# Kernel tuning notes

Measured on AMD Instinct MI355X. Metric: run time of the kernel, lower is better.

Reference implementation:

```python
import jax, jax.numpy as jnp
import numpy as np

N = 100000
E = 1600000
IN_DIM, HID, OUT, HEADS, EDGE_DIM = 64, 32, 32, 4, 1


def setup_inputs() -> dict:
    key = jax.random.key(0)
    ks = jax.random.split(key, 24)
    p = lambda k, shape: (jax.random.normal(k, shape, dtype=jnp.float32) * 0.1)
    inp = {
        "x": jax.random.normal(ks[0], (N, IN_DIM), dtype=jnp.float32),
        "edge_index": jax.random.randint(ks[1], (2, E), 0, N, dtype=jnp.int32),
        "edge_attr": jax.random.uniform(ks[2], (E, EDGE_DIM), dtype=jnp.float32),
        # BatchNorm1d(edge_dim), eval mode
        "bn_gamma": jnp.ones((EDGE_DIM,), jnp.float32),
        "bn_beta": jnp.zeros((EDGE_DIM,), jnp.float32),
        "bn_mean": jnp.zeros((EDGE_DIM,), jnp.float32),
        "bn_var": jnp.ones((EDGE_DIM,), jnp.float32),
        # GATConv layer 1: in_dim -> hidden, heads=4, concat
        "W1": p(ks[3], (IN_DIM, HEADS * HID)),
        "as1": p(ks[4], (HEADS, HID)),
        "ad1": p(ks[5], (HEADS, HID)),
        "We1": p(ks[6], (EDGE_DIM, HEADS * HID)),
        "ae1": p(ks[7], (HEADS, HID)),
        "b1": jnp.zeros((HEADS * HID,), jnp.float32),
        # GATConv layer 2: heads*hidden -> out, heads=1, no concat
        "W2": p(ks[8], (HEADS * HID, OUT)),
        "as2": p(ks[9], (1, OUT)),
        "ad2": p(ks[10], (1, OUT)),
        "We2": p(ks[11], (EDGE_DIM, OUT)),
        "ae2": p(ks[12], (1, OUT)),
        "b2": jnp.zeros((OUT,), jnp.float32),
        # feature decoder MLP
        "Wd1": p(ks[13], (OUT, HID)),
        "bd1": jnp.zeros((HID,), jnp.float32),
        "Wd2": p(ks[14], (HID, IN_DIM)),
        "bd2": jnp.zeros((IN_DIM,), jnp.float32),
    }
    return inp


def gat_layer(x, src, dst, e, W, a_src, a_dst, We, a_e, b, heads, out_ch, concat):
    n = x.shape[0]
    h = (x @ W).reshape(n, heads, out_ch)                     # [N,H,C]
    alpha_src = (h * a_src).sum(-1)                           # [N,H]
    alpha_dst = (h * a_dst).sum(-1)                           # [N,H]
    he = (e @ We).reshape(-1, heads, out_ch)                  # [E,H,C]
    alpha = alpha_src[src] + alpha_dst[dst] + (he * a_e).sum(-1)  # [E,H]
    alpha = jax.nn.leaky_relu(alpha, 0.2)
    # segment softmax over destination node
    amax = jax.ops.segment_max(alpha, dst, num_segments=n)
    amax = jnp.where(jnp.isfinite(amax), amax, 0.0)
    ex = jnp.exp(alpha - amax[dst])
    denom = jax.ops.segment_sum(ex, dst, num_segments=n)
    att = ex / (denom[dst] + 1e-16)                           # [E,H]
    msg = h[src] * att[:, :, None]                            # [E,H,C]
    out = jax.ops.segment_sum(msg, dst, num_segments=n)       # [N,H,C]
    out = out.reshape(n, heads * out_ch) if concat else out.mean(axis=1)
    return out + b


def reference(x, edge_index, edge_attr, bn_gamma, bn_beta, bn_mean, bn_var,
              W1, as1, ad1, We1, ae1, b1, W2, as2, ad2, We2, ae2, b2,
              Wd1, bd1, Wd2, bd2):
    src, dst = edge_index[0], edge_index[1]
    # edge_norm(log1p(edge_attr)) with BatchNorm1d in eval mode
    e = (jnp.log1p(edge_attr) - bn_mean) * jax.lax.rsqrt(bn_var + 1e-5) * bn_gamma + bn_beta
    # encoder (dropout inactive in eval)
    h = gat_layer(x, src, dst, e, W1, as1, ad1, We1, ae1, b1, HEADS, HID, True)
    h = jax.nn.elu(h)
    z = gat_layer(h, src, dst, e, W2, as2, ad2, We2, ae2, b2, 1, OUT, False)
    # feature decoder MLP
    x_hat = jax.nn.elu(z @ Wd1 + bd1) @ Wd2 + bd2
    return (z, x_hat)
```

## Files before the change

### kernel.cpp

```cpp
#include <hip/hip_runtime.h>
#include <hip/hip_fp16.h>
#include <math.h>

#define NN 100000
#define NE 1600000

typedef _Float16 h2v __attribute__((ext_vector_type(2)));
__device__ __forceinline__ float fdot2f(__half2 a, __half2 b, float c) {
#if __has_builtin(__builtin_amdgcn_fdot2)
    return __builtin_amdgcn_fdot2(*(h2v*)&a, *(h2v*)&b, c, false);
#else
    c = fmaf(__half2float(__low2half(a)),  __half2float(__low2half(b)),  c);
    c = fmaf(__half2float(__high2half(a)), __half2float(__high2half(b)), c);
    return c;
#endif
}

__global__ void k_hist(const int* __restrict__ ei, int* __restrict__ counts,
                       int* __restrict__ rank) {
    int e = blockIdx.x * blockDim.x + threadIdx.x;
    if (e < NE) rank[e] = atomicAdd(&counts[ei[NE + e]], 1);
}

__global__ void k_s1(const int* __restrict__ counts, int* __restrict__ bsum) {
    __shared__ int sd[256];
    int tid = threadIdx.x, b = blockIdx.x;
    int base = b * 2048 + tid * 8;
    int s = 0;
    #pragma unroll
    for (int j = 0; j < 8; ++j) {
        int g = base + j;
        s += (g < NN) ? counts[g] : 0;
    }
    sd[tid] = s;
    __syncthreads();
    for (int d = 128; d; d >>= 1) {
        if (tid < d) sd[tid] += sd[tid + d];
        __syncthreads();
    }
    if (tid == 0) bsum[b] = sd[0];
}

__global__ void k_s2(const int* __restrict__ bsum, int* __restrict__ boff,
                     int* __restrict__ rowptr,
                     const float* __restrict__ We1, const float* __restrict__ ae1,
                     const float* __restrict__ We2, const float* __restrict__ ae2,
                     float* __restrict__ wdot) {
    int t = threadIdx.x;
    if (t == 0) {
        int run = 0;
        for (int b = 0; b < 49; ++b) { boff[b] = run; run += bsum[b]; }
        rowptr[NN] = NE;
    }
    if (t >= 64 && t < 68) {
        int h = t - 64;
        float s = 0.f;
        for (int c = 0; c < 32; ++c) s += We1[h*32+c] * ae1[h*32+c];
        wdot[h] = s;
    } else if (t == 68) {
        float s = 0.f;
        for (int c = 0; c < 32; ++c) s += We2[c] * ae2[c];
        wdot[4] = s;
    }
}

__global__ void k_s3(const int* __restrict__ counts, const int* __restrict__ boff,
                     int* __restrict__ rowptr) {
    __shared__ int sT[256];
    int tid = threadIdx.x, b = blockIdx.x;
    int base = b * 2048 + tid * 8;
    int c[8];
    int s = 0;
    #pragma unroll
    for (int j = 0; j < 8; ++j) {
        int g = base + j;
        c[j] = (g < NN) ? counts[g] : 0;
        s += c[j];
    }
    sT[tid] = s;
    __syncthreads();
    for (int d = 1; d < 256; d <<= 1) {
        int v = (tid >= d) ? sT[tid - d] : 0;
        __syncthreads();
        sT[tid] += v;
        __syncthreads();
    }
    int run = (tid ? sT[tid - 1] : 0) + boff[b];
    #pragma unroll
    for (int j = 0; j < 8; ++j) {
        int g = base + j;
        if (g < NN) rowptr[g] = run;
        run += c[j];
    }
}

__global__ void __launch_bounds__(256, 2)
k1_node1(const float* __restrict__ x, const float* __restrict__ W1,
         const float* __restrict__ as1, const float* __restrict__ ad1,
         __half2* __restrict__ h1h, float* __restrict__ as1n,
         float* __restrict__ ad1n) {
    int tid = threadIdx.x, wid = tid >> 6, lane = tid & 63;
    float wc0[64], wc1[64];
    #pragma unroll
    for (int k = 0; k < 64; ++k) {
        wc0[k] = W1[k*128 + 2*lane];
        wc1[k] = W1[k*128 + 2*lane + 1];
    }
    float asc0 = as1[2*lane], asc1 = as1[2*lane+1];
    float adc0 = ad1[2*lane], adc1 = ad1[2*lane+1];
    int gw = (blockIdx.x << 2) + wid;
    int nw = gridDim.x << 2;
    for (int n = gw; n < NN; n += nw) {
        int nu = __builtin_amdgcn_readfirstlane(n);
        const float* xr = x + (size_t)nu * 64;
        float a0 = 0.f, a1 = 0.f;
        #pragma unroll
        for (int k = 0; k < 64; ++k) {
            float xk = xr[k];
            a0 = fmaf(xk, wc0[k], a0);
            a1 = fmaf(xk, wc1[k], a1);
        }
        h1h[(size_t)nu*64 + lane] = __float22half2_rn(make_float2(a0, a1));
        float p = a0*asc0 + a1*asc1;
        float q = a0*adc0 + a1*adc1;
        #pragma unroll
        for (int d = 1; d < 16; d <<= 1) {
            p += __shfl_xor(p, d);
            q += __shfl_xor(q, d);
        }
        if ((lane & 15) == 0) {
            int h = lane >> 4;
            as1n[nu*4 + h] = p;
            ad1n[nu*4 + h] = q;
        }
    }
}

__global__ void k_scatter(const int* __restrict__ ei, const float* __restrict__ ea,
                          const float* __restrict__ g, const float* __restrict__ b,
                          const float* __restrict__ m, const float* __restrict__ v,
                          const int* __restrict__ rowptr, const int* __restrict__ rank,
                          const float* __restrict__ as1n, const float* __restrict__ ad1n,
                          const float* __restrict__ wdot, int4* __restrict__ rec) {
    int e = blockIdx.x * blockDim.x + threadIdx.x;
    if (e >= NE) return;
    int src = ei[e], dst = ei[NE + e];
    int pos = rowptr[dst] + rank[e];
    float en = (log1pf(ea[e]) - m[0]) * rsqrtf(v[0] + 1e-5f) * g[0] + b[0];
    float4 wd  = *(const float4*)wdot;
    float4 asv = *(const float4*)&as1n[src*4];
    float4 adv = *(const float4*)&ad1n[dst*4];
    float a0 = asv.x + adv.x + en*wd.x; a0 = fmaxf(a0, 0.2f*a0);
    float a1 = asv.y + adv.y + en*wd.y; a1 = fmaxf(a1, 0.2f*a1);
    float a2 = asv.z + adv.z + en*wd.z; a2 = fmaxf(a2, 0.2f*a2);
    float a3 = asv.w + adv.w + en*wd.w; a3 = fmaxf(a3, 0.2f*a3);
    __half2 p01 = __floats2half2_rn(__expf(a0), __expf(a1));
    __half2 p23 = __floats2half2_rn(__expf(a2), __expf(a3));
    int4 rc;
    rc.x = src;
    rc.y = __float_as_int(en);
    rc.z = *(const int*)&p01;
    rc.w = *(const int*)&p23;
    rec[pos] = rc;
}

__global__ void __launch_bounds__(256)
kA1(const int* __restrict__ rowptr, const int4* __restrict__ rec,
    const __half2* __restrict__ h1h,
    const float* __restrict__ b1, const float* __restrict__ W2,
    const float* __restrict__ as2, const float* __restrict__ ad2,
    __half2* __restrict__ h2h, float* __restrict__ as2n, float* __restrict__ ad2n) {
    __shared__ __half2 W2h[64*32];
    __shared__ float4 exs4[4][64];
    __shared__ int    srcl[4][64];
    __shared__ __half2 slot_h2[4][64];
    int tid = threadIdx.x, wid = tid >> 6, lane = tid & 63;
    for (int i = tid; i < 2048; i += 256) {
        int k2 = i >> 5, c = i & 31;
        W2h[i] = __floats2half2_rn(W2[(2*k2)*32 + c], W2[(2*k2+1)*32 + c]);
    }
    __syncthreads();

    int n = blockIdx.x * 4 + wid;
    int row0 = rowptr[n], row1 = rowptr[n + 1];
    int es4 = lane >> 4;
    int co  = lane & 15;
    int hq4 = co >> 2;
    float den0 = 0.f, den1 = 0.f, den2 = 0.f, den3 = 0.f;
    float acc[8] = {0.f,0.f,0.f,0.f,0.f,0.f,0.f,0.f};
    const float* exf = (const float*)&exs4[wid][0];
    const uint4* h1u4 = (const uint4*)h1h;

    for (int base = row0; base < row1; base += 64) {
        int j = base + lane;
        bool val = j < row1;
        int4 rc = val ? rec[j] : make_int4(0, 0, 0, 0);
        float2 e01 = __half22float2(*(const __half2*)&rc.z);
        float2 e23 = __half22float2(*(const __half2*)&rc.w);
        den0 += e01.x; den1 += e01.y; den2 += e23.x; den3 += e23.y;
        exs4[wid][lane] = make_float4(e01.x, e01.y, e23.x, e23.y);
        srcl[wid][lane] = rc.x;

        int cnt = min(64, row1 - base);
        int i = 0;
        for (; i + 4 < cnt; i += 8) {
            int idxA = i + es4, idxB = i + 4 + es4;
            int sA = srcl[wid][idxA];
            int sB = srcl[wid][idxB];
            float exA = exf[idxA*4 + hq4];
            float exB = exf[idxB*4 + hq4];
            uint4 uA = h1u4[(size_t)sA*16 + co];
            uint4 uB = h1u4[(size_t)sB*16 + co];
            __half2 a01 = *(const __half2*)&uA.x, a23 = *(const __half2*)&uA.y;
            __half2 a45 = *(const __half2*)&uA.z, a67 = *(const __half2*)&uA.w;
            acc[0] = fmaf(exA, __half2float(__low2half(a01)),  acc[0]);
            acc[1] = fmaf(exA, __half2float(__high2half(a01)), acc[1]);
            acc[2] = fmaf(exA, __half2float(__low2half(a23)),  acc[2]);
            acc[3] = fmaf(exA, __half2float(__high2half(a23)), acc[3]);
            acc[4] = fmaf(exA, __half2float(__low2half(a45)),  acc[4]);
            acc[5] = fmaf(exA, __half2float(__high2half(a45)), acc[5]);
            acc[6] = fmaf(exA, __half2float(__low2half(a67)),  acc[6]);
            acc[7] = fmaf(exA, __half2float(__high2half(a67)), acc[7]);
            __half2 b01 = *(const __half2*)&uB.x, b23 = *(const __half2*)&uB.y;
            __half2 b45 = *(const __half2*)&uB.z, b67 = *(const __half2*)&uB.w;
            acc[0] = fmaf(exB, __half2float(__low2half(b01)),  acc[0]);
            acc[1] = fmaf(exB, __half2float(__high2half(b01)), acc[1]);
            acc[2] = fmaf(exB, __half2float(__low2half(b23)),  acc[2]);
            acc[3] = fmaf(exB, __half2float(__high2half(b23)), acc[3]);
            acc[4] = fmaf(exB, __half2float(__low2half(b45)),  acc[4]);
            acc[5] = fmaf(exB, __half2float(__high2half(b45)), acc[5]);
            acc[6] = fmaf(exB, __half2float(__low2half(b67)),  acc[6]);
            acc[7] = fmaf(exB, __half2float(__high2half(b67)), acc[7]);
        }
        if (i < cnt) {
            int idx = i + es4;
            int s = srcl[wid][idx];
            float ex = exf[idx*4 + hq4];
            uint4 u = h1u4[(size_t)s*16 + co];
            __half2 h01 = *(const __half2*)&u.x, h23 = *(const __half2*)&u.y;
            __half2 h45 = *(const __half2*)&u.z, h67 = *(const __half2*)&u.w;
            acc[0] = fmaf(ex, __half2float(__low2half(h01)),  acc[0]);
            acc[1] = fmaf(ex, __half2float(__high2half(h01)), acc[1]);
            acc[2] = fmaf(ex, __half2float(__low2half(h23)),  acc[2]);
            acc[3] = fmaf(ex, __half2float(__high2half(h23)), acc[3]);
            acc[4] = fmaf(ex, __half2float(__low2half(h45)),  acc[4]);
            acc[5] = fmaf(ex, __half2float(__high2half(h45)), acc[5]);
            acc[6] = fmaf(ex, __half2float(__low2half(h67)),  acc[6]);
            acc[7] = fmaf(ex, __half2float(__high2half(h67)), acc[7]);
        }
    }
    #pragma unroll
    for (int k = 0; k < 8; ++k) {
        acc[k] += __shfl_xor(acc[k], 16);
        acc[k] += __shfl_xor(acc[k], 32);
    }
    #pragma unroll
    for (int d = 32; d; d >>= 1) {
        den0 += __shfl_xor(den0, d); den1 += __shfl_xor(den1, d);
        den2 += __shfl_xor(den2, d); den3 += __shfl_xor(den3, d);
    }
    float dh = (hq4 == 0) ? den0 : (hq4 == 1) ? den1 : (hq4 == 2) ? den2 : den3;
    float r = 1.f / (dh + 1e-16f);
    float accA = (es4 == 0) ? acc[0] : (es4 == 1) ? acc[2] : (es4 == 2) ? acc[4] : acc[6];
    float accB = (es4 == 0) ? acc[1] : (es4 == 1) ? acc[3] : (es4 == 2) ? acc[5] : acc[7];
    int cp = 4*co + es4;
    float2 bb = ((const float2*)b1)[cp];
    float oA = accA * r + bb.x;
    float oB = accB * r + bb.y;
    oA = oA > 0.f ? oA : __expf(oA) - 1.f;
    oB = oB > 0.f ? oB : __expf(oB) - 1.f;
    slot_h2[wid][cp] = __floats2half2_rn(oA, oB);

    int es = lane >> 5, cq = lane & 31;
    int k2base = es * 32;
    float s2 = 0.f;
    #pragma unroll
    for (int kk = 0; kk < 32; ++kk)
        s2 = fdot2f(slot_h2[wid][k2base + kk], W2h[(k2base + kk)*32 + cq], s2);
    s2 += __shfl_xor(s2, 32);
    int l4 = lane & 15;
    float za = __shfl(s2, 2*l4);
    float zb = __shfl(s2, 2*l4 + 1);
    if (lane < 16) h2h[(size_t)n*16 + l4] = __float22half2_rn(make_float2(za, zb));
    float av = s2 * as2[cq] * 0.5f;
    float dv = s2 * ad2[cq] * 0.5f;
    #pragma unroll
    for (int d = 32; d; d >>= 1) { av += __shfl_xor(av, d); dv += __shfl_xor(dv, d); }
    if (lane == 0) { as2n[n] = av; ad2n[n] = dv; }
}

__global__ void __launch_bounds__(256)
kA2(const int* __restrict__ rowptr, const int4* __restrict__ rec,
    const float* __restrict__ as2n, const float* __restrict__ ad2n,
    const float* __restrict__ wdot, const __half2* __restrict__ h2h,
    const float* __restrict__ b2, const float* __restrict__ Wd1,
    const float* __restrict__ bd1, const float* __restrict__ Wd2,
    const float* __restrict__ bd2, float* __restrict__ out) {
    __shared__ __half2 Wd1h[16*32];
    __shared__ __half2 Wd2h[16*64];
    __shared__ float pl[4][64];
    __shared__ int   srcl[4][64];
    __shared__ __half2 zh2[4][16], th2[4][16];
    int tid = threadIdx.x, wid = tid >> 6, lane = tid & 63;
    int es8 = lane >> 3, l3 = lane & 7;
    int half = lane >> 5, l5 = lane & 31;
    int l4 = lane & 15;
    for (int i = tid; i < 512; i += 256) {
        int kp = i >> 5, c = i & 31;
        Wd1h[i] = __floats2half2_rn(Wd1[(2*kp)*32 + c], Wd1[(2*kp+1)*32 + c]);
    }
    for (int i = tid; i < 1024; i += 256) {
        int kp = i >> 6, c = i & 63;
        Wd2h[i] = __floats2half2_rn(Wd2[(2*kp)*64 + c], Wd2[(2*kp+1)*64 + c]);
    }
    __syncthreads();

    int n = blockIdx.x * 4 + wid;
    int row0 = rowptr[n], row1 = rowptr[n + 1];
    float wd4 = wdot[4];
    float adn = ad2n[n];
    float den = 0.f;
    float acc[4] = {0.f, 0.f, 0.f, 0.f};
    const uint2* h2u2 = (const uint2*)h2h;

    for (int base = row0; base < row1; base += 64) {
        int j = base + lane;
        bool val = j < row1;
        int4 rc = val ? rec[j] : make_int4(0, 0, 0, 0);
        int sv = rc.x;
        float en = __int_as_float(rc.y);
        float a = as2n[sv] + adn + en * wd4;
        a = fmaxf(a, 0.2f*a);
        float p = val ? __expf(a) : 0.f;
        den += p;
        pl[wid][lane] = p;
        srcl[wid][lane] = sv;

        int cnt = min(64, row1 - base);
        int i = 0;
        for (; i + 8 < cnt; i += 16) {
            int idxA = i + es8, idxB = i + 8 + es8;
            int sA = srcl[wid][idxA];
            int sB = srcl[wid][idxB];
            float exA = pl[wid][idxA];
            float exB = pl[wid][idxB];
            uint2 uA = h2u2[(size_t)sA*8 + l3];
            uint2 uB = h2u2[(size_t)sB*8 + l3];
            __half2 a01 = *(const __half2*)&uA.x, a23 = *(const __half2*)&uA.y;
            acc[0] = fmaf(exA, __half2float(__low2half(a01)),  acc[0]);
            acc[1] = fmaf(exA, __half2float(__high2half(a01)), acc[1]);
            acc[2] = fmaf(exA, __half2float(__low2half(a23)),  acc[2]);
            acc[3] = fmaf(exA, __half2float(__high2half(a23)), acc[3]);
            __half2 b01 = *(const __half2*)&uB.x, b23 = *(const __half2*)&uB.y;
            acc[0] = fmaf(exB, __half2float(__low2half(b01)),  acc[0]);
            acc[1] = fmaf(exB, __half2float(__high2half(b01)), acc[1]);
            acc[2] = fmaf(exB, __half2float(__low2half(b23)),  acc[2]);
            acc[3] = fmaf(exB, __half2float(__high2half(b23)), acc[3]);
        }
        if (i < cnt) {
            int idx = i + es8;
            int se = srcl[wid][idx];
            float ex = pl[wid][idx];
            uint2 u = h2u2[(size_t)se*8 + l3];
            __half2 h01 = *(const __half2*)&u.x, h23 = *(const __half2*)&u.y;
            acc[0] = fmaf(ex, __half2float(__low2half(h01)),  acc[0]);
            acc[1] = fmaf(ex, __half2float(__high2half(h01)), acc[1]);
            acc[2] = fmaf(ex, __half2float(__low2half(h23)),  acc[2]);
            acc[3] = fmaf(ex, __half2float(__high2half(h23)), acc[3]);
        }
    }
    #pragma unroll
    for (int d = 32; d; d >>= 1) den += __shfl_xor(den, d);
    #pragma unroll
    for (int k = 0; k < 4; ++k) {
        acc[k] += __shfl_xor(acc[k], 8);
        acc[k] += __shfl_xor(acc[k], 16);
        acc[k] += __shfl_xor(acc[k], 32);
    }
    float r = 1.f / (den + 1e-16f);
    if (lane < 8) {
        float4 b2v = ((const float4*)b2)[l3];
        float z0 = acc[0]*r + b2v.x;
        float z1 = acc[1]*r + b2v.y;
        float z2 = acc[2]*r + b2v.z;
        float z3 = acc[3]*r + b2v.w;
        *(float4*)&out[(size_t)n*32 + 4*l3] = make_float4(z0, z1, z2, z3);
        zh2[wid][2*l3]     = __floats2half2_rn(z0, z1);
        zh2[wid][2*l3 + 1] = __floats2half2_rn(z2, z3);
    }

    int kp0 = half * 8;
    float t2 = 0.f;
    #pragma unroll
    for (int k = 0; k < 8; ++k)
        t2 = fdot2f(zh2[wid][kp0 + k], Wd1h[(kp0 + k)*32 + l5], t2);
    t2 += __shfl_xor(t2, 32);
    t2 += bd1[l5];
    t2 = t2 > 0.f ? t2 : __expf(t2) - 1.f;
    float ta = __shfl(t2, 2*l4);
    float tb = __shfl(t2, 2*l4 + 1);
    if (lane < 16) th2[wid][l4] = __floats2half2_rn(ta, tb);

    float xo = bd2[lane];
    #pragma unroll
    for (int k = 0; k < 16; ++k)
        xo = fdot2f(th2[wid][k], Wd2h[k*64 + lane], xo);
    out[(size_t)NN*32 + (size_t)n*64 + lane] = xo;
}

extern "C" void kernel_launch(void* const* d_in, const int* in_sizes, int n_in,
                              void* d_out, int out_size, void* d_ws, size_t ws_size,
                              hipStream_t stream) {
    const float* x    = (const float*)d_in[0];
    const int*   ei   = (const int*)  d_in[1];
    const float* ea   = (const float*)d_in[2];
    const float* bng  = (const float*)d_in[3];
    const float* bnb  = (const float*)d_in[4];
    const float* bnm  = (const float*)d_in[5];
    const float* bnv  = (const float*)d_in[6];
    const float* W1   = (const float*)d_in[7];
    const float* as1  = (const float*)d_in[8];
    const float* ad1  = (const float*)d_in[9];
    const float* We1  = (const float*)d_in[10];
    const float* ae1  = (const float*)d_in[11];
    const float* b1   = (const float*)d_in[12];
    const float* W2   = (const float*)d_in[13];
    const float* as2  = (const float*)d_in[14];
    const float* ad2  = (const float*)d_in[15];
    const float* We2  = (const float*)d_in[16];
    const float* ae2  = (const float*)d_in[17];
    const float* b2   = (const float*)d_in[18];
    const float* Wd1  = (const float*)d_in[19];
    const float* bd1  = (const float*)d_in[20];
    const float* Wd2  = (const float*)d_in[21];
    const float* bd2  = (const float*)d_in[22];
    float* out = (float*)d_out;

    char* wsb = (char*)d_ws;
    __half2* h1h = (__half2*)wsb;
    float* as1n  = (float*)(wsb += (size_t)NN*64*4);
    float* ad1n  = (float*)(wsb += (size_t)NN*4*4);
    __half2* h2h = (__half2*)(wsb += (size_t)NN*4*4);
    float* as2n  = (float*)(wsb += (size_t)NN*16*4);
    float* ad2n  = (float*)(wsb += (size_t)NN*4);
    float* wdot  = (float*)(wsb += (size_t)NN*4);
    int4* rec    = (int4*)(wsb += 8*4);
    int* rank    = (int*)(wsb += (size_t)NE*16);
    int* counts  = (int*)(wsb += (size_t)NE*4);
    int* rowptr  = (int*)(wsb += (size_t)NN*4);
    int* bsum    = (int*)(wsb += (size_t)(NN+1)*4);
    int* boff    = (int*)(wsb += 64*4);

    hipMemsetAsync(counts, 0, NN * sizeof(int), stream);
    hipLaunchKernelGGL(k_hist, dim3((NE+255)/256), dim3(256), 0, stream, ei, counts, rank);
    hipLaunchKernelGGL(k_s1, dim3(49), dim3(256), 0, stream, counts, bsum);
    hipLaunchKernelGGL(k_s2, dim3(1), dim3(128), 0, stream,
                       bsum, boff, rowptr, We1, ae1, We2, ae2, wdot);
    hipLaunchKernelGGL(k_s3, dim3(49), dim3(256), 0, stream, counts, boff, rowptr);
    hipLaunchKernelGGL(k1_node1, dim3(1024), dim3(256), 0, stream,
                       x, W1, as1, ad1, h1h, as1n, ad1n);
    hipLaunchKernelGGL(k_scatter, dim3((NE+255)/256), dim3(256), 0, stream,
                       ei, ea, bng, bnb, bnm, bnv, rowptr, rank,
                       as1n, ad1n, wdot, rec);
    hipLaunchKernelGGL(kA1, dim3(NN/4), dim3(256), 0, stream,
                       rowptr, rec, h1h, b1, W2, as2, ad2, h2h, as2n, ad2n);
    hipLaunchKernelGGL(kA2, dim3(NN/4), dim3(256), 0, stream,
                       rowptr, rec, as2n, ad2n, wdot, h2h, b2, Wd1, bd1, Wd2, bd2,
                       out);
}
```

Measured before the change: 368.2 us.

## Slice layer-1 aggregation by channel group to shrink the gathered working set

```diff
diff --git a/kernel.cpp b/kernel.cpp
--- a/kernel.cpp
+++ b/kernel.cpp
@@ -97,7 +97,7 @@
 __global__ void __launch_bounds__(256, 2)
 k1_node1(const float* __restrict__ x, const float* __restrict__ W1,
          const float* __restrict__ as1, const float* __restrict__ ad1,
-         __half2* __restrict__ h1h, float* __restrict__ as1n,
+         __half2* __restrict__ h1g, float* __restrict__ as1n,
          float* __restrict__ ad1n) {
     int tid = threadIdx.x, wid = tid >> 6, lane = tid & 63;
     float wc0[64], wc1[64];
@@ -108,6 +108,7 @@
     }
     float asc0 = as1[2*lane], asc1 = as1[2*lane+1];
     float adc0 = ad1[2*lane], adc1 = ad1[2*lane+1];
+    size_t gslice = (size_t)(lane >> 3) * NN * 8 + (lane & 7);
     int gw = (blockIdx.x << 2) + wid;
     int nw = gridDim.x << 2;
     for (int n = gw; n < NN; n += nw) {
@@ -120,7 +121,7 @@
             a0 = fmaf(xk, wc0[k], a0);
             a1 = fmaf(xk, wc1[k], a1);
         }
-        h1h[(size_t)nu*64 + lane] = __float22half2_rn(make_float2(a0, a1));
+        h1g[gslice + (size_t)nu*8] = __float22half2_rn(make_float2(a0, a1));
         float p = a0*asc0 + a1*asc1;
         float q = a0*adc0 + a1*adc1;
         #pragma unroll
@@ -164,15 +165,113 @@
     rec[pos] = rc;
 }
 
+__global__ void k_repack(const int4* __restrict__ rec, int* __restrict__ srcp,
+                         __half* __restrict__ exps) {
+    int j = blockIdx.x * blockDim.x + threadIdx.x;
+    if (j >= NE) return;
+    int4 rc = rec[j];
+    srcp[j] = rc.x;
+    __half2 p01 = *(const __half2*)&rc.z;
+    __half2 p23 = *(const __half2*)&rc.w;
+    exps[j]               = __low2half(p01);
+    exps[NE + j]          = __high2half(p01);
+    exps[2*(size_t)NE + j] = __low2half(p23);
+    exps[3*(size_t)NE + j] = __high2half(p23);
+}
+
 __global__ void __launch_bounds__(256)
-kA1(const int* __restrict__ rowptr, const int4* __restrict__ rec,
-    const __half2* __restrict__ h1h,
-    const float* __restrict__ b1, const float* __restrict__ W2,
+kA1s(const int* __restrict__ rowptr, const int* __restrict__ srcp,
+     const __half* __restrict__ exps, const uint4* __restrict__ h1g,
+     const float* __restrict__ b1, __half2* __restrict__ out1h2) {
+    __shared__ int   srcl[4][64];
+    __shared__ float exl[4][64];
+    __shared__ float accl[4][16];
+    int tid = threadIdx.x, wid = tid >> 6, lane = tid & 63;
+    int g = blockIdx.x & 7;
+    int n = (blockIdx.x >> 3) * 4 + wid;
+    int hh = g >> 1;
+    const __half* expsH = exps + (size_t)hh * NE;
+    const uint4* hg = h1g + (size_t)g * NN * 2;
+    int row0 = rowptr[n], row1 = rowptr[n + 1];
+    int es = lane >> 1, cl = lane & 1;
+    float den = 0.f;
+    float acc[8] = {0.f,0.f,0.f,0.f,0.f,0.f,0.f,0.f};
+
+    for (int base = row0; base < row1; base += 64) {
+        int j = base + lane;
+        bool val = j < row1;
+        int s = val ? srcp[j] : 0;
+        float ex = val ? __half2float(expsH[j]) : 0.f;
+        den += ex;
+        srcl[wid][lane] = s;
+        exl[wid][lane]  = ex;
+
+        int cnt = min(64, row1 - base);
+        {
+            int sA = srcl[wid][es];
+            float exA = exl[wid][es];
+            uint4 u = hg[(size_t)sA*2 + cl];
+            __half2 h01 = *(const __half2*)&u.x, h23 = *(const __half2*)&u.y;
+            __half2 h45 = *(const __half2*)&u.z, h67 = *(const __half2*)&u.w;
+            acc[0] = fmaf(exA, __half2float(__low2half(h01)),  acc[0]);
+            acc[1] = fmaf(exA, __half2float(__high2half(h01)), acc[1]);
+            acc[2] = fmaf(exA, __half2float(__low2half(h23)),  acc[2]);
+            acc[3] = fmaf(exA, __half2float(__high2half(h23)), acc[3]);
+            acc[4] = fmaf(exA, __half2float(__low2half(h45)),  acc[4]);
+            acc[5] = fmaf(exA, __half2float(__high2half(h45)), acc[5]);
+            acc[6] = fmaf(exA, __half2float(__low2half(h67)),  acc[6]);
+            acc[7] = fmaf(exA, __half2float(__high2half(h67)), acc[7]);
+        }
+        if (cnt > 32) {
+            int sB = srcl[wid][32 + es];
+            float exB = exl[wid][32 + es];
+            uint4 u = hg[(size_t)sB*2 + cl];
+            __half2 h01 = *(const __half2*)&u.x, h23 = *(const __half2*)&u.y;
+            __half2 h45 = *(const __half2*)&u.z, h67 = *(const __half2*)&u.w;
+            acc[0] = fmaf(exB, __half2float(__low2half(h01)),  acc[0]);
+            acc[1] = fmaf(exB, __half2float(__high2half(h01)), acc[1]);
+            acc[2] = fmaf(exB, __half2float(__low2half(h23)),  acc[2]);
+            acc[3] = fmaf(exB, __half2float(__high2half(h23)), acc[3]);
+            acc[4] = fmaf(exB, __half2float(__low2half(h45)),  acc[4]);
+            acc[5] = fmaf(exB, __half2float(__high2half(h45)), acc[5]);
+            acc[6] = fmaf(exB, __half2float(__low2half(h67)),  acc[6]);
+            acc[7] = fmaf(exB, __half2float(__high2half(h67)), acc[7]);
+        }
+    }
+    #pragma unroll
+    for (int k = 0; k < 8; ++k) {
+        acc[k] += __shfl_xor(acc[k], 2);
+        acc[k] += __shfl_xor(acc[k], 4);
+        acc[k] += __shfl_xor(acc[k], 8);
+        acc[k] += __shfl_xor(acc[k], 16);
+        acc[k] += __shfl_xor(acc[k], 32);
+    }
+    #pragma unroll
+    for (int d = 1; d < 64; d <<= 1) den += __shfl_xor(den, d);
+    if (lane < 2) {
+        #pragma unroll
+        for (int k = 0; k < 8; ++k) accl[wid][lane*8 + k] = acc[k];
+    }
+    if (lane < 8) {
+        int p  = lane >> 2;
+        int i0 = (2*lane) & 7;
+        float vA = accl[wid][p*8 + i0];
+        float vB = accl[wid][p*8 + i0 + 1];
+        float r = 1.f / (den + 1e-16f);
+        float2 bb = ((const float2*)b1)[8*g + lane];
+        float oA = vA * r + bb.x;
+        float oB = vB * r + bb.y;
+        oA = oA > 0.f ? oA : __expf(oA) - 1.f;
+        oB = oB > 0.f ? oB : __expf(oB) - 1.f;
+        out1h2[(size_t)n*64 + g*8 + lane] = __floats2half2_rn(oA, oB);
+    }
+}
+
+__global__ void __launch_bounds__(256)
+kW2(const __half2* __restrict__ out1h2, const float* __restrict__ W2,
     const float* __restrict__ as2, const float* __restrict__ ad2,
     __half2* __restrict__ h2h, float* __restrict__ as2n, float* __restrict__ ad2n) {
     __shared__ __half2 W2h[64*32];
-    __shared__ float4 exs4[4][64];
-    __shared__ int    srcl[4][64];
     __shared__ __half2 slot_h2[4][64];
     int tid = threadIdx.x, wid = tid >> 6, lane = tid & 63;
     for (int i = tid; i < 2048; i += 256) {
@@ -182,94 +281,7 @@
     __syncthreads();
 
     int n = blockIdx.x * 4 + wid;
-    int row0 = rowptr[n], row1 = rowptr[n + 1];
-    int es4 = lane >> 4;
-    int co  = lane & 15;
-    int hq4 = co >> 2;
-    float den0 = 0.f, den1 = 0.f, den2 = 0.f, den3 = 0.f;
-    float acc[8] = {0.f,0.f,0.f,0.f,0.f,0.f,0.f,0.f};
-    const float* exf = (const float*)&exs4[wid][0];
-    const uint4* h1u4 = (const uint4*)h1h;
-
-    for (int base = row0; base < row1; base += 64) {
-        int j = base + lane;
-        bool val = j < row1;
-        int4 rc = val ? rec[j] : make_int4(0, 0, 0, 0);
-        float2 e01 = __half22float2(*(const __half2*)&rc.z);
-        float2 e23 = __half22float2(*(const __half2*)&rc.w);
-        den0 += e01.x; den1 += e01.y; den2 += e23.x; den3 += e23.y;
-        exs4[wid][lane] = make_float4(e01.x, e01.y, e23.x, e23.y);
-        srcl[wid][lane] = rc.x;
-
-        int cnt = min(64, row1 - base);
-        int i = 0;
-        for (; i + 4 < cnt; i += 8) {
-            int idxA = i + es4, idxB = i + 4 + es4;
-            int sA = srcl[wid][idxA];
-            int sB = srcl[wid][idxB];
-            float exA = exf[idxA*4 + hq4];
-            float exB = exf[idxB*4 + hq4];
-            uint4 uA = h1u4[(size_t)sA*16 + co];
-            uint4 uB = h1u4[(size_t)sB*16 + co];
-            __half2 a01 = *(const __half2*)&uA.x, a23 = *(const __half2*)&uA.y;
-            __half2 a45 = *(const __half2*)&uA.z, a67 = *(const __half2*)&uA.w;
-            acc[0] = fmaf(exA, __half2float(__low2half(a01)),  acc[0]);
-            acc[1] = fmaf(exA, __half2float(__high2half(a01)), acc[1]);
-            acc[2] = fmaf(exA, __half2float(__low2half(a23)),  acc[2]);
-            acc[3] = fmaf(exA, __half2float(__high2half(a23)), acc[3]);
-            acc[4] = fmaf(exA, __half2float(__low2half(a45)),  acc[4]);
-            acc[5] = fmaf(exA, __half2float(__high2half(a45)), acc[5]);
-            acc[6] = fmaf(exA, __half2float(__low2half(a67)),  acc[6]);
-            acc[7] = fmaf(exA, __half2float(__high2half(a67)), acc[7]);
-            __half2 b01 = *(const __half2*)&uB.x, b23 = *(const __half2*)&uB.y;
-            __half2 b45 = *(const __half2*)&uB.z, b67 = *(const __half2*)&uB.w;
-            acc[0] = fmaf(exB, __half2float(__low2half(b01)),  acc[0]);
-            acc[1] = fmaf(exB, __half2float(__high2half(b01)), acc[1]);
-            acc[2] = fmaf(exB, __half2float(__low2half(b23)),  acc[2]);
-            acc[3] = fmaf(exB, __half2float(__high2half(b23)), acc[3]);
-            acc[4] = fmaf(exB, __half2float(__low2half(b45)),  acc[4]);
-            acc[5] = fmaf(exB, __half2float(__high2half(b45)), acc[5]);
-            acc[6] = fmaf(exB, __half2float(__low2half(b67)),  acc[6]);
-            acc[7] = fmaf(exB, __half2float(__high2half(b67)), acc[7]);
-        }
-        if (i < cnt) {
-            int idx = i + es4;
-            int s = srcl[wid][idx];
-            float ex = exf[idx*4 + hq4];
-            uint4 u = h1u4[(size_t)s*16 + co];
-            __half2 h01 = *(const __half2*)&u.x, h23 = *(const __half2*)&u.y;
-            __half2 h45 = *(const __half2*)&u.z, h67 = *(const __half2*)&u.w;
-            acc[0] = fmaf(ex, __half2float(__low2half(h01)),  acc[0]);
-            acc[1] = fmaf(ex, __half2float(__high2half(h01)), acc[1]);
-            acc[2] = fmaf(ex, __half2float(__low2half(h23)),  acc[2]);
-            acc[3] = fmaf(ex, __half2float(__high2half(h23)), acc[3]);
-            acc[4] = fmaf(ex, __half2float(__low2half(h45)),  acc[4]);
-            acc[5] = fmaf(ex, __half2float(__high2half(h45)), acc[5]);
-            acc[6] = fmaf(ex, __half2float(__low2half(h67)),  acc[6]);
-            acc[7] = fmaf(ex, __half2float(__high2half(h67)), acc[7]);
-        }
-    }
-    #pragma unroll
-    for (int k = 0; k < 8; ++k) {
-        acc[k] += __shfl_xor(acc[k], 16);
-        acc[k] += __shfl_xor(acc[k], 32);
-    }
-    #pragma unroll
-    for (int d = 32; d; d >>= 1) {
-        den0 += __shfl_xor(den0, d); den1 += __shfl_xor(den1, d);
-        den2 += __shfl_xor(den2, d); den3 += __shfl_xor(den3, d);
-    }
-    float dh = (hq4 == 0) ? den0 : (hq4 == 1) ? den1 : (hq4 == 2) ? den2 : den3;
-    float r = 1.f / (dh + 1e-16f);
-    float accA = (es4 == 0) ? acc[0] : (es4 == 1) ? acc[2] : (es4 == 2) ? acc[4] : acc[6];
-    float accB = (es4 == 0) ? acc[1] : (es4 == 1) ? acc[3] : (es4 == 2) ? acc[5] : acc[7];
-    int cp = 4*co + es4;
-    float2 bb = ((const float2*)b1)[cp];
-    float oA = accA * r + bb.x;
-    float oB = accB * r + bb.y;
-    oA = oA > 0.f ? oA : __expf(oA) - 1.f;
-    oB = oB > 0.f ? oB : __expf(oB) - 1.f;
-    slot_h2[wid][cp] = __floats2half2_rn(oA, oB);
+    slot_h2[wid][lane] = out1h2[(size_t)n*64 + lane];
 
     int es = lane >> 5, cq = lane & 31;
     int k2base = es * 32;
@@ -437,7 +449,7 @@
     float* out = (float*)d_out;
 
     char* wsb = (char*)d_ws;
-    __half2* h1h = (__half2*)wsb;
+    __half2* h1g = (__half2*)wsb;
     float* as1n  = (float*)(wsb += (size_t)NN*64*4);
     float* ad1n  = (float*)(wsb += (size_t)NN*4*4);
     __half2* h2h = (__half2*)(wsb += (size_t)NN*4*4);
@@ -450,6 +462,9 @@
     int* rowptr  = (int*)(wsb += (size_t)NN*4);
     int* bsum    = (int*)(wsb += (size_t)(NN+1)*4);
     int* boff    = (int*)(wsb += 64*4);
+    int* srcp    = (int*)(wsb += 64*4);
+    __half* exps = (__half*)(wsb += (size_t)NE*4);
+    __half2* out1h2 = (__half2*)(wsb += (size_t)NE*4*2);
 
     hipMemsetAsync(counts, 0, NN * sizeof(int), stream);
     hipLaunchKernelGGL(k_hist, dim3((NE+255)/256), dim3(256), 0, stream, ei, counts, rank);
@@ -458,12 +473,16 @@
                        bsum, boff, rowptr, We1, ae1, We2, ae2, wdot);
     hipLaunchKernelGGL(k_s3, dim3(49), dim3(256), 0, stream, counts, boff, rowptr);
     hipLaunchKernelGGL(k1_node1, dim3(1024), dim3(256), 0, stream,
-                       x, W1, as1, ad1, h1h, as1n, ad1n);
+                       x, W1, as1, ad1, h1g, as1n, ad1n);
     hipLaunchKernelGGL(k_scatter, dim3((NE+255)/256), dim3(256), 0, stream,
                        ei, ea, bng, bnb, bnm, bnv, rowptr, rank,
                        as1n, ad1n, wdot, rec);
-    hipLaunchKernelGGL(kA1, dim3(NN/4), dim3(256), 0, stream,
-                       rowptr, rec, h1h, b1, W2, as2, ad2, h2h, as2n, ad2n);
+    hipLaunchKernelGGL(k_repack, dim3((NE+255)/256), dim3(256), 0, stream,
+                       rec, srcp, exps);
+    hipLaunchKernelGGL(kA1s, dim3((NN/4)*8), dim3(256), 0, stream,
+                       rowptr, srcp, exps, (const uint4*)h1g, b1, out1h2);
+    hipLaunchKernelGGL(kW2, dim3(NN/4), dim3(256), 0, stream,
+                       out1h2, W2, as2, ad2, h2h, as2n, ad2n);
     hipLaunchKernelGGL(kA2, dim3(NN/4), dim3(256), 0, stream,
                        rowptr, rec, as2n, ad2n, wdot, h2h, b2, Wd1, bd1, Wd2, bd2,
                        out);
```

Measured after the change: 737.9 us. 2x slower.
